# Optimization experiments

Measured on AMD Instinct MI355X. Metric: run time of the kernel, lower is better.

The kernel has to match this reference:

```python
import jax, jax.numpy as jnp
import numpy as np

N_OUT, N_IN, K = 64, 64, 3


def setup_inputs() -> dict:
    key = jax.random.key(0)
    ks = jax.random.split(key, 6)
    bs, emb_dim, g_latent = 32, 512, 256
    w_flat = N_OUT * N_IN * K * K  # 36864
    return {
        "emb": jax.random.normal(ks[0], (bs, emb_dim), jnp.float32),
        "x": jax.random.normal(ks[1], (bs, N_IN, 96, 96), jnp.float32),
        "w1_w": jax.random.normal(ks[2], (g_latent, emb_dim), jnp.float32) * (1.0 / np.sqrt(emb_dim)),
        "w1_b": jax.random.normal(ks[3], (g_latent,), jnp.float32) * 0.01,
        "w2_w": jax.random.normal(ks[4], (w_flat, g_latent), jnp.float32) * (1.0 / np.sqrt(g_latent)),
        "w2_b": jax.random.normal(ks[5], (w_flat,), jnp.float32) * 0.01,
    }


def reference(emb, x, w1_w, w1_b, w2_w, w2_b):
    bs, c, h, w = x.shape
    # Hypernetwork: Linear -> ReLU -> Linear, predicting per-sample conv weights
    hdn = jax.nn.relu(emb @ w1_w.T + w1_b)                      # [bs, g_latent]
    weights = (hdn @ w2_w.T + w2_b).reshape(bs * N_OUT, N_IN, K, K)
    # Per-sample conv via grouped conv trick: x -> (1, bs*c, h, w), groups=bs
    xtag = x.reshape(1, bs * c, h, w)
    out = jax.lax.conv_general_dilated(
        xtag, weights,
        window_strides=(1, 1), padding=((0, 0), (0, 0)),
        dimension_numbers=("NCHW", "OIHW", "NCHW"),
        feature_group_count=bs,
    )  # [1, bs*N_OUT, h-K+1, w-K+1]
    return out.reshape(bs, N_OUT, out.shape[-2], out.shape[-1])
```

## Files before the change

kernel.cpp:

```cpp
#include <hip/hip_runtime.h>

typedef __attribute__((ext_vector_type(8)))  _Float16 half8;
typedef __attribute__((ext_vector_type(4)))  _Float16 half4;
typedef __attribute__((ext_vector_type(16))) float    f32x16;

#define G_LATENT 256
#define EMB      512
#define WFLAT    36864

__global__ __launch_bounds__(256) void k1_hdn(
    const float* __restrict__ emb, const float* __restrict__ w1w,
    const float* __restrict__ w1b, _Float16* __restrict__ hdn16)
{
    const int s = blockIdx.x;
    const int j = threadIdx.x;
    const float4* e4 = (const float4*)(emb + (size_t)s * EMB);
    const float4* w4 = (const float4*)(w1w + (size_t)j * EMB);
    float a0 = 0.f, a1 = 0.f;
#pragma unroll 8
    for (int k = 0; k < EMB / 4; k += 2) {
        float4 a = e4[k],     b = w4[k];
        float4 c = e4[k + 1], d = w4[k + 1];
        a0 += a.x * b.x + a.y * b.y + a.z * b.z + a.w * b.w;
        a1 += c.x * d.x + c.y * d.y + c.z * d.z + c.w * d.w;
    }
    const float acc = fmaxf(a0 + a1 + w1b[j], 0.f);
    const int kb = j >> 4;
    const int h  = (j >> 2) & 1;
    const int e  = (j & 3) + 4 * ((j >> 3) & 1);
    hdn16[(kb * 64 + s + 32 * h) * 8 + e] = (_Float16)acc;
}

__global__ __launch_bounds__(256) void k2_wfrag(
    const _Float16* __restrict__ hdn16, const float* __restrict__ w2w,
    const float* __restrict__ w2b, _Float16* __restrict__ wfrag)
{
    __shared__ __align__(16) _Float16 sm[8 * 256 * 8];

    const int b     = blockIdx.x;
    const int ihalf = b & 1;
    const int oct   = (b >> 1) & 1;
    const int kbc   = (b >> 2) & 3;
    const int khw   = b >> 4;

    const int t = threadIdx.x, lane = t & 63, wv = t >> 6;
    const int h = lane >> 5, l31 = lane & 31;

    const int oc31 = t & 31, icof = t >> 5;
    const size_t rrow = (size_t)(oct * 32 + oc31) * 576
                      + (size_t)(kbc * 16 + ihalf * 8 + icof) * 9 + khw;
    const float* wrow = w2w + rrow * G_LATENT;

    float bias[2];
#pragma unroll
    for (int ntl = 0; ntl < 2; ++ntl) {
        const int nt = wv * 2 + ntl;
        const size_t rc = (size_t)(oct * 32 + l31) * 576
                        + (size_t)(kbc * 16 + ihalf * 8 + nt) * 9 + khw;
        bias[ntl] = w2b[rc];
    }

    const f32x16 z16 = {0,0,0,0,0,0,0,0,0,0,0,0,0,0,0,0};
    f32x16 acc[2] = {z16, z16};

    float4 ld[2][16];
#pragma unroll
    for (int u = 0; u < 16; ++u) ld[0][u] = ((const float4*)wrow)[u];

    const half8* __restrict__ hfr = (const half8*)hdn16;

#pragma unroll
    for (int kc = 0; kc < 4; ++kc) {
        __syncthreads();
        if (kc < 3) {
            const float4* nxt = (const float4*)(wrow + (kc + 1) * 64);
#pragma unroll
            for (int u = 0; u < 16; ++u) ld[(kc + 1) & 1][u] = nxt[u];
        }
#pragma unroll
        for (int kb16 = 0; kb16 < 4; ++kb16) {
#pragma unroll
            for (int hh = 0; hh < 2; ++hh) {
                const float4 lo = ld[kc & 1][kb16 * 4 + hh];
                const float4 hi = ld[kc & 1][kb16 * 4 + 2 + hh];
                half8 c;
                c[0] = (_Float16)lo.x; c[1] = (_Float16)lo.y;
                c[2] = (_Float16)lo.z; c[3] = (_Float16)lo.w;
                c[4] = (_Float16)hi.x; c[5] = (_Float16)hi.y;
                c[6] = (_Float16)hi.z; c[7] = (_Float16)hi.w;
                *(half8*)&sm[((kb16 * 2 + hh) * 256 + t) * 8] = c;
            }
        }
        __syncthreads();
#pragma unroll
        for (int kb16 = 0; kb16 < 4; ++kb16) {
            const half8 af = hfr[(kc * 4 + kb16) * 64 + lane];
#pragma unroll
            for (int ntl = 0; ntl < 2; ++ntl) {
                const int lr = (wv * 2 + ntl) * 32 + l31;
                const half8 bf = *(const half8*)&sm[((kb16 * 2 + h) * 256 + lr) * 8];
                acc[ntl] = __builtin_amdgcn_mfma_f32_32x32x16_f16(af, bf, acc[ntl], 0, 0, 0);
            }
        }
    }

    __syncthreads();
#pragma unroll
    for (int ntl = 0; ntl < 2; ++ntl) {
        const int nt    = wv * 2 + ntl;
        const int lanep = l31 + 32 * (nt >> 2);
        const int elow  = nt & 3;
#pragma unroll
        for (int g = 0; g < 16; ++g) {
            const int srow = (g & 3) + 8 * (g >> 2) + 4 * h;
            sm[(srow * 64 + lanep) * 4 + elow] = (_Float16)(acc[ntl][g] + bias[ntl]);
        }
    }
    __syncthreads();
#pragma unroll
    for (int i = 0; i < 8; ++i) {
        const int c = t + 256 * i;
        const int s  = c >> 6, lp = c & 63;
        const half4 hv = *(const half4*)&sm[c * 4];
        _Float16* dst = wfrag + ((((size_t)s * 9 + khw) * 4 + kbc) * 2 + oct) * 512
                              + lp * 8 + ihalf * 4;
        *(half4*)dst = hv;
    }
}

__global__ __launch_bounds__(256, 2) void k3_conv(
    const float* __restrict__ x, const _Float16* __restrict__ wfrag,
    float* __restrict__ out)
{
    __shared__ __align__(16) _Float16 lds[14 * 8 * 36 * 8];

    const int b  = blockIdx.x;
    const int wg = (b & 7) * 96 + (b >> 3);
    const int ct = wg % 3;
    const int rt = (wg / 3) & 7;
    const int s  = wg / 24;
    const int rbase  = (rt < 7) ? rt * 12 : 82;
    const int wstart = (ct == 0) ? 0 : (ct == 1) ? 32 : 60;
    const int dlt    = (ct == 2) ? 2 : 0;
    const int tid = threadIdx.x;

    if (tid < 252) {
        const int p9 = tid % 9, q9 = tid / 9;
        const float* xs = x + (size_t)s * 64 * 9216 + (size_t)rbase * 96
                            + wstart + p9 * 4;
#pragma unroll 4
        for (int i = 0; i < 32; ++i) {
            const int piece = q9 + 28 * i;
            const int xr = piece >> 6, ch = piece & 63;
            const float4 v = *(const float4*)(xs + (size_t)ch * 9216 + xr * 96);
            const int kb = ch >> 4, c16 = ch & 15;
            const int hh = (c16 >> 2) & 1;
            const int pz = (c16 & 3) + 4 * ((c16 >> 3) & 1);
            const int base = ((xr * 8 + kb * 2 + hh) * 36 + p9 * 4) * 8 + pz;
            lds[base]      = (_Float16)v.x;
            lds[base + 8]  = (_Float16)v.y;
            lds[base + 16] = (_Float16)v.z;
            lds[base + 24] = (_Float16)v.w;
        }
    }
    __syncthreads();

    const int lane = tid & 63, wv = tid >> 6;
    const int h = lane >> 5, n31 = lane & 31;

    const f32x16 z16 = {0,0,0,0,0,0,0,0,0,0,0,0,0,0,0,0};
    f32x16 acc[2][3];
#pragma unroll
    for (int o = 0; o < 2; ++o)
#pragma unroll
        for (int n = 0; n < 3; ++n) acc[o][n] = z16;

    const half8* __restrict__ A = (const half8*)(wfrag + (size_t)s * WFLAT);

    for (int kh = 0; kh < 3; ++kh) {
        for (int kw = 0; kw < 3; ++kw) {
            const int khw = kh * 3 + kw;
            const int xc  = dlt + n31 + kw;
#pragma unroll
            for (int kb = 0; kb < 4; ++kb) {
                const half8 a0 = A[((khw * 4 + kb) * 2 + 0) * 64 + lane];
                const half8 a1 = A[((khw * 4 + kb) * 2 + 1) * 64 + lane];
#pragma unroll
                for (int n = 0; n < 3; ++n) {
                    const int xr = wv * 3 + n + kh;
                    const half8 bb =
                        *(const half8*)&lds[((xr * 8 + kb * 2 + h) * 36 + xc) * 8];
                    acc[0][n] = __builtin_amdgcn_mfma_f32_32x32x16_f16(a0, bb, acc[0][n], 0, 0, 0);
                    acc[1][n] = __builtin_amdgcn_mfma_f32_32x32x16_f16(a1, bb, acc[1][n], 0, 0, 0);
                }
            }
        }
    }

    const int ocol = wstart + dlt + n31;
#pragma unroll
    for (int ot = 0; ot < 2; ++ot) {
#pragma unroll
        for (int n = 0; n < 3; ++n) {
            const int orow = rbase + wv * 3 + n;
            float* po = out + (size_t)(s * 64 + ot * 32 + 4 * h) * 8836
                            + orow * 94 + ocol;
#pragma unroll
            for (int g = 0; g < 16; ++g) {
                const int od = (g & 3) + 8 * (g >> 2);
                po[(size_t)od * 8836] = acc[ot][n][g];
            }
        }
    }
}

extern "C" void kernel_launch(void* const* d_in, const int* in_sizes, int n_in,
                              void* d_out, int out_size, void* d_ws, size_t ws_size,
                              hipStream_t stream)
{
    (void)in_sizes; (void)n_in; (void)out_size; (void)ws_size;
    const float* emb = (const float*)d_in[0];
    const float* x   = (const float*)d_in[1];
    const float* w1w = (const float*)d_in[2];
    const float* w1b = (const float*)d_in[3];
    const float* w2w = (const float*)d_in[4];
    const float* w2b = (const float*)d_in[5];
    float* out = (float*)d_out;

    _Float16* hdn16 = (_Float16*)d_ws;
    _Float16* wfrag = (_Float16*)((char*)d_ws + 32 * 1024);

    k1_hdn<<<32, 256, 0, stream>>>(emb, w1w, w1b, hdn16);
    k2_wfrag<<<144, 256, 0, stream>>>(hdn16, w2w, w2b, wfrag);
    k3_conv<<<768, 256, 0, stream>>>(x, wfrag, out);
}
```

Before: 227.0 us.

## Retile conv into smaller row tiles with pipelined staging and prefetched weights

The conv kernel moves from 12-row, 768-block tiles to 8-row, 1152-block tiles with occupancy hint 3. The LDS image is 34 columns wide and its staging is restructured into per-thread 8-channel gathers, software-pipelined across 11 iterations. Weight fragments per kernel tap are now register-prefetched one tap ahead. k2 drops its double-buffered global loads for simpler per-chunk loads. The intent is to raise occupancy and overlap global loads with compute, at the cost of more halo re-reads, strided scalar loads, and higher register pressure.

```diff
diff --git a/kernel.cpp b/kernel.cpp
--- a/kernel.cpp
+++ b/kernel.cpp
@@ -62,27 +62,21 @@
 
     const f32x16 z16 = {0,0,0,0,0,0,0,0,0,0,0,0,0,0,0,0};
     f32x16 acc[2] = {z16, z16};
-
-    float4 ld[2][16];
-#pragma unroll
-    for (int u = 0; u < 16; ++u) ld[0][u] = ((const float4*)wrow)[u];
-
     const half8* __restrict__ hfr = (const half8*)hdn16;
 
 #pragma unroll
     for (int kc = 0; kc < 4; ++kc) {
         __syncthreads();
-        if (kc < 3) {
-            const float4* nxt = (const float4*)(wrow + (kc + 1) * 64);
-#pragma unroll
-            for (int u = 0; u < 16; ++u) ld[(kc + 1) & 1][u] = nxt[u];
-        }
+        float4 ld[16];
+        const float4* src = (const float4*)(wrow + kc * 64);
+#pragma unroll
+        for (int u = 0; u < 16; ++u) ld[u] = src[u];
 #pragma unroll
         for (int kb16 = 0; kb16 < 4; ++kb16) {
 #pragma unroll
             for (int hh = 0; hh < 2; ++hh) {
-                const float4 lo = ld[kc & 1][kb16 * 4 + hh];
-                const float4 hi = ld[kc & 1][kb16 * 4 + 2 + hh];
+                const float4 lo = ld[kb16 * 4 + hh];
+                const float4 hi = ld[kb16 * 4 + 2 + hh];
                 half8 c;
                 c[0] = (_Float16)lo.x; c[1] = (_Float16)lo.y;
                 c[2] = (_Float16)lo.z; c[3] = (_Float16)lo.w;
@@ -128,81 +122,103 @@
     }
 }
 
-__global__ __launch_bounds__(256, 2) void k3_conv(
+#define XCOLS 34
+#define NGRP  80
+#define NSLOT (NGRP * XCOLS)
+#define NIT   11
+
+__device__ __forceinline__ void ld_grp(const float* __restrict__ xs, int slot,
+                                       int rbase, float v[8])
+{
+    const int grp = slot / XCOLS;
+    const int col = slot - grp * XCOLS;
+    const int xr  = grp >> 3;
+    const int kb  = (grp >> 1) & 3;
+    const int h   = grp & 1;
+    const int row = min(rbase + xr, 95);
+    const float* p = xs + (size_t)(kb * 16 + 4 * h) * 9216 + row * 96 + col;
+#pragma unroll
+    for (int c = 0; c < 4; ++c) v[c] = p[(size_t)c * 9216];
+#pragma unroll
+    for (int c = 0; c < 4; ++c) v[4 + c] = p[(size_t)(8 + c) * 9216];
+}
+
+__global__ __launch_bounds__(256, 3) void k3_conv(
     const float* __restrict__ x, const _Float16* __restrict__ wfrag,
     float* __restrict__ out)
 {
-    __shared__ __align__(16) _Float16 lds[14 * 8 * 36 * 8];
+    __shared__ __align__(16) half8 lds[NIT * 256];
 
     const int b  = blockIdx.x;
-    const int wg = (b & 7) * 96 + (b >> 3);
+    const int wg = (b & 7) * 144 + (b >> 3);
     const int ct = wg % 3;
-    const int rt = (wg / 3) & 7;
-    const int s  = wg / 24;
-    const int rbase  = (rt < 7) ? rt * 12 : 82;
-    const int wstart = (ct == 0) ? 0 : (ct == 1) ? 32 : 60;
-    const int dlt    = (ct == 2) ? 2 : 0;
+    const int rt = (wg / 3) % 12;
+    const int s  = wg / 36;
+    const int rbase  = (rt < 11) ? rt * 8 : 86;
+    const int cstart = (ct == 0) ? 0 : (ct == 1) ? 32 : 62;
     const int tid = threadIdx.x;
 
-    if (tid < 252) {
-        const int p9 = tid % 9, q9 = tid / 9;
-        const float* xs = x + (size_t)s * 64 * 9216 + (size_t)rbase * 96
-                            + wstart + p9 * 4;
-#pragma unroll 4
-        for (int i = 0; i < 32; ++i) {
-            const int piece = q9 + 28 * i;
-            const int xr = piece >> 6, ch = piece & 63;
-            const float4 v = *(const float4*)(xs + (size_t)ch * 9216 + xr * 96);
-            const int kb = ch >> 4, c16 = ch & 15;
-            const int hh = (c16 >> 2) & 1;
-            const int pz = (c16 & 3) + 4 * ((c16 >> 3) & 1);
-            const int base = ((xr * 8 + kb * 2 + hh) * 36 + p9 * 4) * 8 + pz;
-            lds[base]      = (_Float16)v.x;
-            lds[base + 8]  = (_Float16)v.y;
-            lds[base + 16] = (_Float16)v.z;
-            lds[base + 24] = (_Float16)v.w;
-        }
-    }
-    __syncthreads();
+    const float* xs = x + (size_t)s * 64 * 9216 + cstart;
+
+    float cur[8], nxt[8];
+    ld_grp(xs, tid, rbase, cur);
+#pragma unroll
+    for (int it = 0; it < NIT; ++it) {
+        const int slot = tid + it * 256;
+        if (it + 1 < NIT) ld_grp(xs, slot + 256, rbase, nxt);
+        half8 v;
+#pragma unroll
+        for (int c = 0; c < 8; ++c) v[c] = (_Float16)cur[c];
+        lds[slot] = v;
+#pragma unroll
+        for (int c = 0; c < 8; ++c) cur[c] = nxt[c];
+    }
 
     const int lane = tid & 63, wv = tid >> 6;
     const int h = lane >> 5, n31 = lane & 31;
+    const int row0 = wv * 2;
 
     const f32x16 z16 = {0,0,0,0,0,0,0,0,0,0,0,0,0,0,0,0};
-    f32x16 acc[2][3];
+    f32x16 acc[2][2];
 #pragma unroll
     for (int o = 0; o < 2; ++o)
 #pragma unroll
-        for (int n = 0; n < 3; ++n) acc[o][n] = z16;
+        for (int n = 0; n < 2; ++n) acc[o][n] = z16;
 
     const half8* __restrict__ A = (const half8*)(wfrag + (size_t)s * WFLAT);
-
-    for (int kh = 0; kh < 3; ++kh) {
-        for (int kw = 0; kw < 3; ++kw) {
-            const int khw = kh * 3 + kw;
-            const int xc  = dlt + n31 + kw;
-#pragma unroll
-            for (int kb = 0; kb < 4; ++kb) {
-                const half8 a0 = A[((khw * 4 + kb) * 2 + 0) * 64 + lane];
-                const half8 a1 = A[((khw * 4 + kb) * 2 + 1) * 64 + lane];
-#pragma unroll
-                for (int n = 0; n < 3; ++n) {
-                    const int xr = wv * 3 + n + kh;
-                    const half8 bb =
-                        *(const half8*)&lds[((xr * 8 + kb * 2 + h) * 36 + xc) * 8];
-                    acc[0][n] = __builtin_amdgcn_mfma_f32_32x32x16_f16(a0, bb, acc[0][n], 0, 0, 0);
-                    acc[1][n] = __builtin_amdgcn_mfma_f32_32x32x16_f16(a1, bb, acc[1][n], 0, 0, 0);
-                }
-            }
-        }
-    }
-
-    const int ocol = wstart + dlt + n31;
+    half8 ac[8], an[8];
+#pragma unroll
+    for (int u = 0; u < 8; ++u) ac[u] = A[u * 64 + lane];
+
+    __syncthreads();
+
+#pragma unroll
+    for (int khw = 0; khw < 9; ++khw) {
+        const int kh = khw / 3, kw = khw - kh * 3;
+        if (khw < 8) {
+#pragma unroll
+            for (int u = 0; u < 8; ++u) an[u] = A[((khw + 1) * 8 + u) * 64 + lane];
+        }
+#pragma unroll
+        for (int kb = 0; kb < 4; ++kb) {
+#pragma unroll
+            for (int n = 0; n < 2; ++n) {
+                const int xr = row0 + n + kh;
+                const half8 bb = lds[(xr * 8 + kb * 2 + h) * XCOLS + n31 + kw];
+                acc[0][n] = __builtin_amdgcn_mfma_f32_32x32x16_f16(ac[kb * 2 + 0], bb, acc[0][n], 0, 0, 0);
+                acc[1][n] = __builtin_amdgcn_mfma_f32_32x32x16_f16(ac[kb * 2 + 1], bb, acc[1][n], 0, 0, 0);
+            }
+        }
+#pragma unroll
+        for (int u = 0; u < 8; ++u) ac[u] = an[u];
+    }
+
+    const int ocol = cstart + n31;
 #pragma unroll
     for (int ot = 0; ot < 2; ++ot) {
 #pragma unroll
-        for (int n = 0; n < 3; ++n) {
-            const int orow = rbase + wv * 3 + n;
+        for (int n = 0; n < 2; ++n) {
+            const int orow = rbase + row0 + n;
             float* po = out + (size_t)(s * 64 + ot * 32 + 4 * h) * 8836
                             + orow * 94 + ocol;
 #pragma unroll
@@ -232,5 +248,5 @@
 
     k1_hdn<<<32, 256, 0, stream>>>(emb, w1w, w1b, hdn16);
     k2_wfrag<<<144, 256, 0, stream>>>(hdn16, w2w, w2b, wfrag);
-    k3_conv<<<768, 256, 0, stream>>>(x, wfrag, out);
-}
+    k3_conv<<<1152, 256, 0, stream>>>(x, wfrag, out);
+}
```

Measured after the change: 232.0 us. 2.2% more time.
